# Performance work log

Hardware: AMD Instinct MI355X
Metric: run time of the kernel (lower is better)

Reference implementation:

```python
import jax, jax.numpy as jnp
import numpy as np

D_MODEL = 1024
N_HEADS = 16
D_HEAD = D_MODEL // N_HEADS


def setup_inputs() -> dict:
    key = jax.random.key(0)
    kx, kq, kk, kv, ko = jax.random.split(key, 5)
    s = 1.0 / np.sqrt(D_MODEL)  # ~ nn.Linear init scale
    return {
        "x": jax.random.normal(kx, (2, 2048, D_MODEL), dtype=jnp.float32),
        "Wq": jax.random.uniform(kq, (D_MODEL, D_MODEL), jnp.float32, -s, s),
        "Wk": jax.random.uniform(kk, (D_MODEL, D_MODEL), jnp.float32, -s, s),
        "Wv": jax.random.uniform(kv, (D_MODEL, D_MODEL), jnp.float32, -s, s),
        "Wo": jax.random.uniform(ko, (D_MODEL, D_MODEL), jnp.float32, -s, s),
    }


def reference(x, Wq, Wk, Wv, Wo):
    B, T, D = x.shape
    H, Dh = N_HEADS, D_HEAD
    # nn.Linear computes x @ W.T; project then split heads -> [B,H,T,Dh]
    q = (x @ Wq.T).reshape(B, T, H, Dh).transpose(0, 2, 1, 3)
    k = (x @ Wk.T).reshape(B, T, H, Dh).transpose(0, 2, 1, 3)
    v = (x @ Wv.T).reshape(B, T, H, Dh).transpose(0, 2, 1, 3)
    att = jnp.einsum("bhqd,bhkd->bhqk", q, k) / jnp.sqrt(jnp.float32(Dh))
    causal = jnp.tril(jnp.ones((T, T), dtype=bool))  # True = keep
    att = jnp.where(causal[None, None], att, -jnp.inf)
    w = jax.nn.softmax(att, axis=-1)
    out = jnp.einsum("bhqk,bhkd->bhqd", w, v)
    out = out.transpose(0, 2, 1, 3).reshape(B, T, D)
    return out @ Wo.T
```

## Files before the change

### kernel.cpp

```cpp
#include <hip/hip_runtime.h>
#include <hip/hip_bf16.h>

typedef __bf16 bf16;
typedef __bf16 bf16x4 __attribute__((ext_vector_type(4)));
typedef __bf16 bf16x8 __attribute__((ext_vector_type(8)));
typedef float  f32x4  __attribute__((ext_vector_type(4)));

#define DEV static __device__ __forceinline__

DEV void gload_lds16(const void* g, void* l) {
  __builtin_amdgcn_global_load_lds((const __attribute__((address_space(1))) void*)g,
                                   (__attribute__((address_space(3))) void*)l, 16, 0, 0);
}

DEV f32x4 mfma16(bf16x8 a, bf16x8 b, f32x4 c) {
  return __builtin_amdgcn_mfma_f32_16x16x32_bf16(a, b, c, 0, 0, 0);
}

__global__ void convert_all(const float* __restrict__ x,
                            const float* __restrict__ wq, const float* __restrict__ wk,
                            const float* __restrict__ wv, const float* __restrict__ wo,
                            bf16* __restrict__ xb,
                            bf16* __restrict__ wqb, bf16* __restrict__ wkb,
                            bf16* __restrict__ wvb, bf16* __restrict__ wob) {
  const int NX = 4194304;
  const int NW = 1048576;
  const int total4 = (NX + 4 * NW) / 4;
  for (int i = blockIdx.x * blockDim.x + threadIdx.x; i < total4;
       i += gridDim.x * blockDim.x) {
    int e = i * 4;
    const float* src; bf16* dst; int off;
    if (e < NX) { src = x; dst = xb; off = e; }
    else {
      int r = e - NX; int w = r >> 20; off = r & (NW - 1);
      src = (w == 0) ? wq : (w == 1) ? wk : (w == 2) ? wv : wo;
      dst = (w == 0) ? wqb : (w == 1) ? wkb : (w == 2) ? wvb : wob;
    }
    float4 v = *(const float4*)(src + off);
    bf16x4 o; o[0] = (bf16)v.x; o[1] = (bf16)v.y; o[2] = (bf16)v.z; o[3] = (bf16)v.w;
    *(bf16x4*)(dst + off) = o;
  }
}

DEV void stage_tile64(const bf16* gsrc, int grow0, int gcol0, int ld_elems,
                      bf16* lds, int chunk, int l) {
  const int p = chunk * 1024 + l * 16;
  const int r = p >> 7;
  const int cb = (p & 127) ^ ((r & 7) << 4);
  gload_lds16((const char*)gsrc + ((size_t)(grow0 + r) * ld_elems + gcol0) * 2 + cb,
              (char*)lds + p);
}

__global__ __launch_bounds__(256) void gemm_qkv(const bf16* __restrict__ xb,
                                                const bf16* __restrict__ Wq_,
                                                const bf16* __restrict__ Wk_,
                                                const bf16* __restrict__ Wv_,
                                                bf16* __restrict__ Qg,
                                                bf16* __restrict__ Kg,
                                                bf16* __restrict__ Vtg) {
  const int z = blockIdx.z;
  const bf16* A  = (z == 2) ? Wv_ : xb;
  const bf16* Bw = (z == 0) ? Wq_ : (z == 1) ? Wk_ : xb;
  const int K = 1024;
  __shared__ bf16 As[128 * 64];
  __shared__ bf16 Bs[128 * 64];
  const int tid = threadIdx.x, w = tid >> 6, l = tid & 63;
  const int row0 = (z == 2 ? blockIdx.y : blockIdx.x) * 128;
  const int col0 = (z == 2 ? blockIdx.x : blockIdx.y) * 128;
  const int wr = (w >> 1) * 64, wc = (w & 1) * 64;
  const int lr = l & 15, lg = l >> 4;
  const int cxor = lr & 7;
  f32x4 acc[4][4] = {};

  for (int kt = 0; kt < 16; ++kt) {
    const int k0 = kt * 64;
#pragma unroll
    for (int i = 0; i < 4; ++i) {
      const int chunk = w * 4 + i;
      stage_tile64(A,  row0, k0, K, As, chunk, l);
      stage_tile64(Bw, col0, k0, K, Bs, chunk, l);
    }
    __syncthreads();
    bf16x8 af[4][2], bfr[4][2];
#pragma unroll
    for (int m = 0; m < 4; ++m) {
      const int r = wr + m * 16 + lr;
#pragma unroll
      for (int h = 0; h < 2; ++h)
        af[m][h] = *(const bf16x8*)((char*)As + r * 128 + (((h * 4 + lg) ^ cxor) << 4));
    }
#pragma unroll
    for (int n = 0; n < 4; ++n) {
      const int r = wc + n * 16 + lr;
#pragma unroll
      for (int h = 0; h < 2; ++h)
        bfr[n][h] = *(const bf16x8*)((char*)Bs + r * 128 + (((h * 4 + lg) ^ cxor) << 4));
    }
#pragma unroll
    for (int m = 0; m < 4; ++m)
#pragma unroll
      for (int n = 0; n < 4; ++n) {
        acc[m][n] = mfma16(af[m][0], bfr[n][0], acc[m][n]);
        acc[m][n] = mfma16(af[m][1], bfr[n][1], acc[m][n]);
      }
    __syncthreads();
  }

  if (z == 2) {
#pragma unroll
    for (int m = 0; m < 4; ++m)
#pragma unroll
      for (int n = 0; n < 4; ++n)
#pragma unroll
        for (int e = 0; e < 4; ++e) {
          const int rr = row0 + wr + m * 16 + lg * 4 + e;
          const int cc = col0 + wc + n * 16 + lr;
          const int h = rr >> 6, dh = rr & 63;
          const int b = cc >> 11, t = cc & 2047;
          Vtg[(((size_t)(b * 16 + h) * 64) + dh) * 2048 + t] = (bf16)acc[m][n][e];
        }
  } else {
    const float scl = (z == 0) ? 0.18033688011112042f : 1.0f;
    bf16* out = (z == 0) ? Qg : Kg;
#pragma unroll
    for (int m = 0; m < 4; ++m)
#pragma unroll
      for (int n = 0; n < 4; ++n)
#pragma unroll
        for (int e = 0; e < 4; ++e) {
          const int r = row0 + wr + m * 16 + lg * 4 + e;
          const int c = col0 + wc + n * 16 + lr;
          const int b = r >> 11, t = r & 2047;
          const int h = c >> 6,  dh = c & 63;
          out[(((size_t)(b * 16 + h) * 2048) + t) * 64 + dh] = (bf16)(acc[m][n][e] * scl);
        }
  }
}

__global__ __launch_bounds__(256) void attn(const bf16* __restrict__ Qg,
                                            const bf16* __restrict__ Kg,
                                            const bf16* __restrict__ Vtg,
                                            bf16* __restrict__ Obt) {
  const int id  = blockIdx.y * 16 + blockIdx.x;
  const int swz = (id & 7) * 64 + (id >> 3);
  const int bh  = swz >> 4;
  const int x   = swz & 15;
  const int tid = threadIdx.x, w = tid >> 6, l = tid & 63;
  const int lr = l & 15, lg = l >> 4;
  __shared__ bf16 Ks[2][8192];
  __shared__ bf16 Vs[2][8192];
  __shared__ bf16 Ps[4][2048];
  const size_t base = (size_t)bh * 2048 * 64;
  const char* kbase = (const char*)(Kg + base);
  const char* vbase = (const char*)(Vtg + base);

  const int rA0 = x * 64 + w * 16;
  const int rB0 = (31 - x) * 64 + w * 16;

  bf16x8 qA[2], qB[2];
  {
    const bf16* qp = Qg + base + (size_t)(rA0 + lr) * 64;
    qA[0] = *(const bf16x8*)(qp + lg * 8);
    qA[1] = *(const bf16x8*)(qp + 32 + lg * 8);
    const bf16* qq = Qg + base + (size_t)(rB0 + lr) * 64;
    qB[0] = *(const bf16x8*)(qq + lg * 8);
    qB[1] = *(const bf16x8*)(qq + 32 + lg * 8);
  }
  f32x4 oA[4] = {}, oB[4] = {};
  f32x4 lA = {}, lB = {};

  bf16x8 ones;
#pragma unroll
  for (int j = 0; j < 8; ++j) ones[j] = (bf16)1.0f;

  const int cxor = lr & 7;

  auto stage = [&](int kt, int buf) {
#pragma unroll
    for (int i = 0; i < 4; ++i) {
      const int p = (w * 4 + i) * 1024 + l * 16;
      const int swk = p ^ (((p >> 7) & 7) << 4);
      gload_lds16(kbase + (size_t)kt * 16384 + swk, (char*)Ks[buf] + p);
      const int vrow = p >> 8;
      const int vcol = (p & 255) ^ (((p >> 8) & 7) << 4);
      gload_lds16(vbase + (size_t)vrow * 4096 + kt * 256 + vcol,
                  (char*)Vs[buf] + p);
    }
  };

  auto computeTile = [&](int kt, int buf, int myrow0, bf16x8 (&qf)[2],
                         f32x4 (&acco)[4], f32x4& lacc) {
    const int k0 = kt * 128;
    const bool full = (k0 + 127 <= myrow0);
    f32x4 accs[8] = {};
    __builtin_amdgcn_s_setprio(1);
#pragma unroll
    for (int n = 0; n < 8; ++n) {
      const int r = n * 16 + lr;
      bf16x8 kf0 = *(const bf16x8*)((char*)Ks[buf] + r * 128 + ((lg ^ cxor) << 4));
      bf16x8 kf1 = *(const bf16x8*)((char*)Ks[buf] + r * 128 + (((4 + lg) ^ cxor) << 4));
      accs[n] = mfma16(kf0, qf[0], accs[n]);
      accs[n] = mfma16(kf1, qf[1], accs[n]);
    }
    __builtin_amdgcn_s_setprio(0);
    if (!full) {
      const int q = myrow0 + lr;
#pragma unroll
      for (int n = 0; n < 8; ++n) {
        const int keyb = k0 + n * 16 + lg * 4;
#pragma unroll
        for (int e = 0; e < 4; ++e)
          if (keyb + e > q) accs[n][e] = -__builtin_inff();
      }
    }
#pragma unroll
    for (int n = 0; n < 8; ++n)
#pragma unroll
      for (int e = 0; e < 4; ++e) accs[n][e] = exp2f(accs[n][e]);
#pragma unroll
    for (int n = 0; n < 8; ++n) {
      bf16x4 p4;
#pragma unroll
      for (int e = 0; e < 4; ++e) p4[e] = (bf16)accs[n][e];
      const int off = (lr * 256 + (n * 16 + lg * 4) * 2) ^ ((lr & 7) << 4);
      *(bf16x4*)((char*)Ps[w] + off) = p4;
    }
    __builtin_amdgcn_s_setprio(1);
#pragma unroll
    for (int c = 0; c < 4; ++c) {
      bf16x8 pf = *(const bf16x8*)((char*)Ps[w] +
                    (lr * 256 + (((c * 4 + lg) ^ cxor) << 4)));
      lacc = mfma16(pf, ones, lacc);
#pragma unroll
      for (int n = 0; n < 4; ++n) {
        const int r = n * 16 + lr;
        bf16x8 vf = *(const bf16x8*)((char*)Vs[buf] +
                      (r * 256 + (((c * 4 + lg) ^ cxor) << 4)));
        acco[n] = mfma16(pf, vf, acco[n]);
      }
    }
    __builtin_amdgcn_s_setprio(0);
  };

  const int nkt   = ((31 - x) >> 1) + 1;
  const int lastA = x >> 1;
  stage(0, 0);
  int cur = 0;
  for (int kt = 0; kt < nkt; ++kt) {
    __syncthreads();
    if (kt + 1 < nkt) stage(kt + 1, cur ^ 1);
    if (kt <= lastA)
      computeTile(kt, cur, rA0, qA, oA, lA);
    computeTile(kt, cur, rB0, qB, oB, lB);
    cur ^= 1;
  }

  const int b = bh >> 4, h = bh & 15;
  f32x4 invA, invB;
#pragma unroll
  for (int e = 0; e < 4; ++e) {
    invA[e] = __builtin_amdgcn_rcpf(lA[e]);
    invB[e] = __builtin_amdgcn_rcpf(lB[e]);
  }
#pragma unroll
  for (int n = 0; n < 4; ++n)
#pragma unroll
    for (int e = 0; e < 4; ++e) {
      const int rA = rA0 + lg * 4 + e;
      Obt[((size_t)(b * 2048 + rA)) * 1024 + h * 64 + n * 16 + lr] = (bf16)(oA[n][e] * invA[e]);
      const int rB = rB0 + lg * 4 + e;
      Obt[((size_t)(b * 2048 + rB)) * 1024 + h * 64 + n * 16 + lr] = (bf16)(oB[n][e] * invB[e]);
    }
}

__global__ __launch_bounds__(256) void gemm_out(const bf16* __restrict__ A,
                                                const bf16* __restrict__ Bw,
                                                float* __restrict__ Cout) {
  const int K = 1024;
  __shared__ bf16 As[128 * 64];
  __shared__ bf16 Bs[64 * 64];
  const int tid = threadIdx.x, w = tid >> 6, l = tid & 63;
  const int row0 = blockIdx.x * 128, col0 = blockIdx.y * 64;
  const int wr = (w >> 1) * 64, wc = (w & 1) * 32;
  const int lr = l & 15, lg = l >> 4;
  const int cxor = lr & 7;
  f32x4 acc[4][2] = {};

  for (int kt = 0; kt < 16; ++kt) {
    const int k0 = kt * 64;
#pragma unroll
    for (int i = 0; i < 4; ++i)
      stage_tile64(A, row0, k0, K, As, w * 4 + i, l);
#pragma unroll
    for (int i = 0; i < 2; ++i)
      stage_tile64(Bw, col0, k0, K, Bs, w * 2 + i, l);
    __syncthreads();
    bf16x8 af[4][2], bfr[2][2];
#pragma unroll
    for (int m = 0; m < 4; ++m) {
      const int r = wr + m * 16 + lr;
#pragma unroll
      for (int h = 0; h < 2; ++h)
        af[m][h] = *(const bf16x8*)((char*)As + r * 128 + (((h * 4 + lg) ^ cxor) << 4));
    }
#pragma unroll
    for (int n = 0; n < 2; ++n) {
      const int r = wc + n * 16 + lr;
#pragma unroll
      for (int h = 0; h < 2; ++h)
        bfr[n][h] = *(const bf16x8*)((char*)Bs + r * 128 + (((h * 4 + lg) ^ cxor) << 4));
    }
#pragma unroll
    for (int m = 0; m < 4; ++m)
#pragma unroll
      for (int n = 0; n < 2; ++n) {
        acc[m][n] = mfma16(af[m][0], bfr[n][0], acc[m][n]);
        acc[m][n] = mfma16(af[m][1], bfr[n][1], acc[m][n]);
      }
    __syncthreads();
  }

#pragma unroll
  for (int m = 0; m < 4; ++m)
#pragma unroll
    for (int n = 0; n < 2; ++n)
#pragma unroll
      for (int e = 0; e < 4; ++e) {
        const int r = row0 + wr + m * 16 + lg * 4 + e;
        const int c = col0 + wc + n * 16 + lr;
        Cout[(size_t)r * 1024 + c] = acc[m][n][e];
      }
}

extern "C" void kernel_launch(void* const* d_in, const int* in_sizes, int n_in,
                              void* d_out, int out_size, void* d_ws, size_t ws_size,
                              hipStream_t stream) {
  const float* x  = (const float*)d_in[0];
  const float* wq = (const float*)d_in[1];
  const float* wk = (const float*)d_in[2];
  const float* wv = (const float*)d_in[3];
  const float* wo = (const float*)d_in[4];
  float* out = (float*)d_out;

  bf16* xb  = (bf16*)d_ws;
  bf16* wqb = xb  + 4194304;
  bf16* wkb = wqb + 1048576;
  bf16* wvb = wkb + 1048576;
  bf16* wob = wvb + 1048576;
  bf16* Qg  = wob + 1048576;
  bf16* Kg  = Qg  + 4194304;
  bf16* Vtg = Kg  + 4194304;
  bf16* Obt = Vtg + 4194304;

  convert_all<<<2048, 256, 0, stream>>>(x, wq, wk, wv, wo, xb, wqb, wkb, wvb, wob);
  gemm_qkv<<<dim3(32, 8, 3), 256, 0, stream>>>(xb, wqb, wkb, wvb, Qg, Kg, Vtg);
  attn<<<dim3(16, 32), 256, 0, stream>>>(Qg, Kg, Vtg, Obt);
  gemm_out<<<dim3(32, 16), 256, 0, stream>>>(Obt, wob, out);
}
```

Baseline: 106.4 us.

## Restructure attention to read K/V from global directly with smaller blocks

The attention kernel drops the LDS double-buffered K/V staging and __syncthreads, and loads K and V fragments straight from global memory (relying on L2/L1). Blocks shrink to 128 threads (2 waves), each wave handling 32 query rows, and the paired light/heavy query-tile load balancing is replaced by one tile per block with heavy tiles scheduled first. This removes block-level sync and LDS traffic and raises occupancy, but trades them for uncoalesced, redundant global/L2 reads of K and V and loses the cross-wave reuse that the shared tile gave.

```diff
diff --git a/kernel.cpp b/kernel.cpp
--- a/kernel.cpp
+++ b/kernel.cpp
@@ -137,140 +137,108 @@
   }
 }
 
-__global__ __launch_bounds__(256) void attn(const bf16* __restrict__ Qg,
+__global__ __launch_bounds__(128) void attn(const bf16* __restrict__ Qg,
                                             const bf16* __restrict__ Kg,
                                             const bf16* __restrict__ Vtg,
                                             bf16* __restrict__ Obt) {
-  const int id  = blockIdx.y * 16 + blockIdx.x;
-  const int swz = (id & 7) * 64 + (id >> 3);
-  const int bh  = swz >> 4;
-  const int x   = swz & 15;
+  const int id  = blockIdx.x;
+  const int swz = (id & 7) * 128 + (id >> 3);
+  const int bh  = swz >> 5;
+  const int x   = 31 - (swz & 31);
   const int tid = threadIdx.x, w = tid >> 6, l = tid & 63;
   const int lr = l & 15, lg = l >> 4;
-  __shared__ bf16 Ks[2][8192];
-  __shared__ bf16 Vs[2][8192];
-  __shared__ bf16 Ps[4][2048];
+  __shared__ bf16 Ps[2][4096];
   const size_t base = (size_t)bh * 2048 * 64;
-  const char* kbase = (const char*)(Kg + base);
-  const char* vbase = (const char*)(Vtg + base);
-
-  const int rA0 = x * 64 + w * 16;
-  const int rB0 = (31 - x) * 64 + w * 16;
-
-  bf16x8 qA[2], qB[2];
-  {
-    const bf16* qp = Qg + base + (size_t)(rA0 + lr) * 64;
-    qA[0] = *(const bf16x8*)(qp + lg * 8);
-    qA[1] = *(const bf16x8*)(qp + 32 + lg * 8);
-    const bf16* qq = Qg + base + (size_t)(rB0 + lr) * 64;
-    qB[0] = *(const bf16x8*)(qq + lg * 8);
-    qB[1] = *(const bf16x8*)(qq + 32 + lg * 8);
-  }
-  f32x4 oA[4] = {}, oB[4] = {};
-  f32x4 lA = {}, lB = {};
-
+  const char* kb = (const char*)(Kg + base);
+  const char* vb = (const char*)(Vtg + base);
+  const int r0 = x * 64 + w * 32;
+
+  bf16x8 qf[2][2];
+#pragma unroll
+  for (int f = 0; f < 2; ++f)
+#pragma unroll
+    for (int h = 0; h < 2; ++h)
+      qf[f][h] = *(const bf16x8*)(Qg + base + (size_t)(r0 + f * 16 + lr) * 64 + h * 32 + lg * 8);
+
+  f32x4 o[2][4] = {};
+  f32x4 lacc[2] = {};
   bf16x8 ones;
 #pragma unroll
   for (int j = 0; j < 8; ++j) ones[j] = (bf16)1.0f;
-
   const int cxor = lr & 7;
-
-  auto stage = [&](int kt, int buf) {
-#pragma unroll
-    for (int i = 0; i < 4; ++i) {
-      const int p = (w * 4 + i) * 1024 + l * 16;
-      const int swk = p ^ (((p >> 7) & 7) << 4);
-      gload_lds16(kbase + (size_t)kt * 16384 + swk, (char*)Ks[buf] + p);
-      const int vrow = p >> 8;
-      const int vcol = (p & 255) ^ (((p >> 8) & 7) << 4);
-      gload_lds16(vbase + (size_t)vrow * 4096 + kt * 256 + vcol,
-                  (char*)Vs[buf] + p);
-    }
-  };
-
-  auto computeTile = [&](int kt, int buf, int myrow0, bf16x8 (&qf)[2],
-                         f32x4 (&acco)[4], f32x4& lacc) {
+  const int nkt = (x >> 1) + 1;
+
+  for (int kt = 0; kt < nkt; ++kt) {
     const int k0 = kt * 128;
-    const bool full = (k0 + 127 <= myrow0);
-    f32x4 accs[8] = {};
+    f32x4 accs[2][8] = {};
     __builtin_amdgcn_s_setprio(1);
 #pragma unroll
     for (int n = 0; n < 8; ++n) {
-      const int r = n * 16 + lr;
-      bf16x8 kf0 = *(const bf16x8*)((char*)Ks[buf] + r * 128 + ((lg ^ cxor) << 4));
-      bf16x8 kf1 = *(const bf16x8*)((char*)Ks[buf] + r * 128 + (((4 + lg) ^ cxor) << 4));
-      accs[n] = mfma16(kf0, qf[0], accs[n]);
-      accs[n] = mfma16(kf1, qf[1], accs[n]);
+      const char* kp = kb + (size_t)(k0 + n * 16 + lr) * 128 + lg * 16;
+      bf16x8 kf0 = *(const bf16x8*)kp;
+      bf16x8 kf1 = *(const bf16x8*)(kp + 64);
+      accs[0][n] = mfma16(kf0, qf[0][0], accs[0][n]);
+      accs[0][n] = mfma16(kf1, qf[0][1], accs[0][n]);
+      accs[1][n] = mfma16(kf0, qf[1][0], accs[1][n]);
+      accs[1][n] = mfma16(kf1, qf[1][1], accs[1][n]);
     }
     __builtin_amdgcn_s_setprio(0);
-    if (!full) {
-      const int q = myrow0 + lr;
+#pragma unroll
+    for (int f = 0; f < 2; ++f) {
+      const int rf = r0 + f * 16;
+      if (k0 + 127 > rf) {
+        const int q = rf + lr;
+#pragma unroll
+        for (int n = 0; n < 8; ++n) {
+          const int keyb = k0 + n * 16 + lg * 4;
+#pragma unroll
+          for (int e = 0; e < 4; ++e)
+            if (keyb + e > q) accs[f][n][e] = -__builtin_inff();
+        }
+      }
 #pragma unroll
       for (int n = 0; n < 8; ++n) {
-        const int keyb = k0 + n * 16 + lg * 4;
-#pragma unroll
-        for (int e = 0; e < 4; ++e)
-          if (keyb + e > q) accs[n][e] = -__builtin_inff();
-      }
-    }
-#pragma unroll
-    for (int n = 0; n < 8; ++n)
-#pragma unroll
-      for (int e = 0; e < 4; ++e) accs[n][e] = exp2f(accs[n][e]);
-#pragma unroll
-    for (int n = 0; n < 8; ++n) {
-      bf16x4 p4;
-#pragma unroll
-      for (int e = 0; e < 4; ++e) p4[e] = (bf16)accs[n][e];
-      const int off = (lr * 256 + (n * 16 + lg * 4) * 2) ^ ((lr & 7) << 4);
-      *(bf16x4*)((char*)Ps[w] + off) = p4;
+        bf16x4 p4;
+#pragma unroll
+        for (int e = 0; e < 4; ++e) p4[e] = (bf16)exp2f(accs[f][n][e]);
+        const int off = ((f * 16 + lr) * 256 + (n * 16 + lg * 4) * 2) ^ ((lr & 7) << 4);
+        *(bf16x4*)((char*)Ps[w] + off) = p4;
+      }
     }
     __builtin_amdgcn_s_setprio(1);
 #pragma unroll
     for (int c = 0; c < 4; ++c) {
-      bf16x8 pf = *(const bf16x8*)((char*)Ps[w] +
-                    (lr * 256 + (((c * 4 + lg) ^ cxor) << 4)));
-      lacc = mfma16(pf, ones, lacc);
+      const int po = ((c * 4 + lg) ^ cxor) << 4;
+      bf16x8 pf0 = *(const bf16x8*)((char*)Ps[w] + lr * 256 + po);
+      bf16x8 pf1 = *(const bf16x8*)((char*)Ps[w] + (16 + lr) * 256 + po);
+      lacc[0] = mfma16(pf0, ones, lacc[0]);
+      lacc[1] = mfma16(pf1, ones, lacc[1]);
 #pragma unroll
       for (int n = 0; n < 4; ++n) {
-        const int r = n * 16 + lr;
-        bf16x8 vf = *(const bf16x8*)((char*)Vs[buf] +
-                      (r * 256 + (((c * 4 + lg) ^ cxor) << 4)));
-        acco[n] = mfma16(pf, vf, acco[n]);
+        bf16x8 vf = *(const bf16x8*)(vb + (size_t)(n * 16 + lr) * 4096 +
+                                     k0 * 2 + c * 64 + lg * 16);
+        o[0][n] = mfma16(pf0, vf, o[0][n]);
+        o[1][n] = mfma16(pf1, vf, o[1][n]);
       }
     }
     __builtin_amdgcn_s_setprio(0);
-  };
-
-  const int nkt   = ((31 - x) >> 1) + 1;
-  const int lastA = x >> 1;
-  stage(0, 0);
-  int cur = 0;
-  for (int kt = 0; kt < nkt; ++kt) {
-    __syncthreads();
-    if (kt + 1 < nkt) stage(kt + 1, cur ^ 1);
-    if (kt <= lastA)
-      computeTile(kt, cur, rA0, qA, oA, lA);
-    computeTile(kt, cur, rB0, qB, oB, lB);
-    cur ^= 1;
-  }
-
-  const int b = bh >> 4, h = bh & 15;
-  f32x4 invA, invB;
-#pragma unroll
-  for (int e = 0; e < 4; ++e) {
-    invA[e] = __builtin_amdgcn_rcpf(lA[e]);
-    invB[e] = __builtin_amdgcn_rcpf(lB[e]);
-  }
-#pragma unroll
-  for (int n = 0; n < 4; ++n)
-#pragma unroll
-    for (int e = 0; e < 4; ++e) {
-      const int rA = rA0 + lg * 4 + e;
-      Obt[((size_t)(b * 2048 + rA)) * 1024 + h * 64 + n * 16 + lr] = (bf16)(oA[n][e] * invA[e]);
-      const int rB = rB0 + lg * 4 + e;
-      Obt[((size_t)(b * 2048 + rB)) * 1024 + h * 64 + n * 16 + lr] = (bf16)(oB[n][e] * invB[e]);
-    }
+  }
+
+  const int b = bh >> 4, hh = bh & 15;
+#pragma unroll
+  for (int f = 0; f < 2; ++f) {
+    f32x4 inv;
+#pragma unroll
+    for (int e = 0; e < 4; ++e) inv[e] = __builtin_amdgcn_rcpf(lacc[f][e]);
+#pragma unroll
+    for (int n = 0; n < 4; ++n)
+#pragma unroll
+      for (int e = 0; e < 4; ++e) {
+        const int r = r0 + f * 16 + lg * 4 + e;
+        Obt[((size_t)(b * 2048 + r)) * 1024 + hh * 64 + n * 16 + lr] =
+            (bf16)(o[f][n][e] * inv[e]);
+      }
+  }
 }
 
 __global__ __launch_bounds__(256) void gemm_out(const bf16* __restrict__ A,
@@ -354,6 +322,6 @@
 
   convert_all<<<2048, 256, 0, stream>>>(x, wq, wk, wv, wo, xb, wqb, wkb, wvb, wob);
   gemm_qkv<<<dim3(32, 8, 3), 256, 0, stream>>>(xb, wqb, wkb, wvb, Qg, Kg, Vtg);
-  attn<<<dim3(16, 32), 256, 0, stream>>>(Qg, Kg, Vtg, Obt);
+  attn<<<1024, 128, 0, stream>>>(Qg, Kg, Vtg, Obt);
   gemm_out<<<dim3(32, 16), 256, 0, stream>>>(Obt, wob, out);
 }
```

New measurement: 176.9 us. 1.66x slower.
